# Optimization experiments

Hardware: AMD Instinct MI355X
Metric: run time of the kernel (lower is better)

## Reference

```python
import jax, jax.numpy as jnp
import numpy as np

N, E = 50000, 800000
NDIM_IN, EDIM, HID, NDIM_OUT, NCLS = 64, 64, 128, 128, 10


def _linear_params(k, fan_in, fan_out):
    lim = 1.0 / np.sqrt(fan_in)
    kw, kb = jax.random.split(k)
    W = jax.random.uniform(kw, (fan_in, fan_out), minval=-lim, maxval=lim, dtype=jnp.float32)
    b = jax.random.uniform(kb, (fan_out,), minval=-lim, maxval=lim, dtype=jnp.float32)
    return W, b


def setup_inputs() -> dict:
    key = jax.random.key(0)
    ks = jax.random.split(key, 9)
    Wm1, bm1 = _linear_params(ks[0], NDIM_IN + EDIM, HID)      # layer1 W_msg
    Wa1, ba1 = _linear_params(ks[1], NDIM_IN + HID, HID)       # layer1 W_apply
    Wm2, bm2 = _linear_params(ks[2], HID + EDIM, NDIM_OUT)     # layer2 W_msg
    Wa2, ba2 = _linear_params(ks[3], HID + NDIM_OUT, NDIM_OUT) # layer2 W_apply
    Wp, bp = _linear_params(ks[4], 2 * NDIM_OUT, NCLS)         # edge predictor
    nfeats = jax.random.normal(ks[5], (N, NDIM_IN), dtype=jnp.float32)
    efeats = jax.random.normal(ks[6], (E, EDIM), dtype=jnp.float32)
    src = jax.random.randint(ks[7], (E,), 0, N)
    dst = jax.random.randint(ks[8], (E,), 0, N)
    return dict(nfeats=nfeats, efeats=efeats, src=src, dst=dst,
                Wm1=Wm1, bm1=bm1, Wa1=Wa1, ba1=ba1,
                Wm2=Wm2, bm2=bm2, Wa2=Wa2, ba2=ba2, Wp=Wp, bp=bp)


def _sage_layer(h, efeats, src, dst, Wm, bm, Wa, ba):
    # per-edge message: W_msg([h_src || e])
    m = jnp.concatenate([h[src], efeats], axis=1) @ Wm + bm          # [E, out]
    # mean aggregation by destination node (0 for zero in-degree, as in DGL fn.mean)
    s = jax.ops.segment_sum(m, dst, num_segments=N)                  # [N, out]
    deg = jax.ops.segment_sum(jnp.ones((E,), m.dtype), dst, num_segments=N)
    h_neigh = s / jnp.maximum(deg, 1.0)[:, None]
    return jax.nn.relu(jnp.concatenate([h, h_neigh], axis=1) @ Wa + ba)


def reference(nfeats, efeats, src, dst, Wm1, bm1, Wa1, ba1, Wm2, bm2, Wa2, ba2, Wp, bp):
    h = _sage_layer(nfeats, efeats, src, dst, Wm1, bm1, Wa1, ba1)
    # dropout between layers is identity in eval mode
    h = _sage_layer(h, efeats, src, dst, Wm2, bm2, Wa2, ba2)
    # MLPPredictor: per-edge score = W([h_u || h_v])
    score = jnp.concatenate([h[src], h[dst]], axis=1) @ Wp + bp      # [E, 10]
    return score
```

## Files before the change

kernel.cpp:

```cpp
#include <hip/hip_runtime.h>

typedef float  f32x4 __attribute__((ext_vector_type(4)));
typedef short  s16x8 __attribute__((ext_vector_type(8)));
typedef unsigned int u32x4 __attribute__((ext_vector_type(4)));

#define DEVINL __device__ __forceinline__

DEVINL float4 ld4(const float* p) { return *reinterpret_cast<const float4*>(p); }
DEVINL void st4(float* p, float4 v) { *reinterpret_cast<float4*>(p) = v; }
DEVINL f32x4 ld4v(const float* p) { return *reinterpret_cast<const f32x4*>(p); }
DEVINL f32x4 ld4nt(const float* p) {
  return __builtin_nontemporal_load(reinterpret_cast<const f32x4*>(p));
}

DEVINL void split8(const float4& f0, const float4& f1, s16x8& hi, s16x8& lo) {
  unsigned hb[8], lb[8];
  const float f[8] = {f0.x, f0.y, f0.z, f0.w, f1.x, f1.y, f1.z, f1.w};
  #pragma unroll
  for (int j = 0; j < 8; ++j) {
    unsigned u = __float_as_uint(f[j]);
    unsigned h = u & 0xffff0000u;
    float l = f[j] - __uint_as_float(h);
    hb[j] = h;
    lb[j] = __float_as_uint(l) & 0xffff0000u;
  }
  u32x4 H = {(hb[0] >> 16) | hb[1], (hb[2] >> 16) | hb[3],
             (hb[4] >> 16) | hb[5], (hb[6] >> 16) | hb[7]};
  u32x4 L = {(lb[0] >> 16) | lb[1], (lb[2] >> 16) | lb[3],
             (lb[4] >> 16) | lb[5], (lb[6] >> 16) | lb[7]};
  hi = __builtin_bit_cast(s16x8, H);
  lo = __builtin_bit_cast(s16x8, L);
}

DEVINL void split1(float f, unsigned short& h, unsigned short& l) {
  unsigned u = __float_as_uint(f);
  unsigned hb = (u + 0x7fffu + ((u >> 16) & 1u)) >> 16;
  float hf = __uint_as_float(hb << 16);
  float d = f - hf;
  unsigned v = __float_as_uint(d);
  unsigned lb = (v + 0x7fffu + ((v >> 16) & 1u)) >> 16;
  h = (unsigned short)hb;
  l = (unsigned short)lb;
}

__global__ __launch_bounds__(128) void wprep2_kernel(
    const float* __restrict__ Wm1, const float* __restrict__ Wa1, const float* __restrict__ bm1,
    const float* __restrict__ Wm2, const float* __restrict__ Wa2, const float* __restrict__ bm2,
    float* __restrict__ bmw1, float* __restrict__ bmw2,
    unsigned short* __restrict__ w1h, unsigned short* __restrict__ w1l,
    unsigned short* __restrict__ w2h, unsigned short* __restrict__ w2l)
{
  int b = blockIdx.x, j = threadIdx.x;
  unsigned short h, l;
  if (b < 128) {
    float acc = 0.f;
    for (int k = 0; k < 128; ++k) acc = fmaf(Wm1[b * 128 + k], Wa1[(64 + k) * 128 + j], acc);
    split1(acc, h, l);
    w1h[(size_t)j * 192 + 64 + b] = h;
    w1l[(size_t)j * 192 + 64 + b] = l;
  } else if (b < 320) {
    int i = b - 128;
    float acc = 0.f;
    for (int k = 0; k < 128; ++k) acc = fmaf(Wm2[i * 128 + k], Wa2[(128 + k) * 128 + j], acc);
    split1(acc, h, l);
    w2h[(size_t)j * 320 + 128 + i] = h;
    w2l[(size_t)j * 320 + 128 + i] = l;
  } else if (b == 320) {
    float acc = 0.f;
    for (int k = 0; k < 128; ++k) acc = fmaf(bm1[k], Wa1[(64 + k) * 128 + j], acc);
    bmw1[j] = acc;
  } else if (b == 321) {
    float acc = 0.f;
    for (int k = 0; k < 128; ++k) acc = fmaf(bm2[k], Wa2[(128 + k) * 128 + j], acc);
    bmw2[j] = acc;
  } else if (b < 386) {
    int t = b - 322;
    split1(Wa1[t * 128 + j], h, l);
    w1h[(size_t)j * 192 + t] = h;
    w1l[(size_t)j * 192 + t] = l;
  } else {
    int t = b - 386;
    split1(Wa2[t * 128 + j], h, l);
    w2h[(size_t)j * 320 + t] = h;
    w2l[(size_t)j * 320 + t] = l;
  }
}

__global__ __launch_bounds__(256) void hist_kernel(
    const int* __restrict__ dst, int* __restrict__ deg, int E)
{
  int e = blockIdx.x * 256 + threadIdx.x;
  if (e < E) atomicAdd(&deg[dst[e]], 1);
}

__global__ __launch_bounds__(256) void scan_blk_kernel(
    const int* __restrict__ in, int* __restrict__ excl, int* __restrict__ bsum, int n)
{
  __shared__ int tmp[256];
  int t = threadIdx.x;
  int i = blockIdx.x * 256 + t;
  int v = (i < n) ? in[i] : 0;
  tmp[t] = v;
  __syncthreads();
  #pragma unroll
  for (int off = 1; off < 256; off <<= 1) {
    int add = (t >= off) ? tmp[t - off] : 0;
    __syncthreads();
    tmp[t] += add;
    __syncthreads();
  }
  if (i < n) excl[i] = tmp[t] - v;
  if (t == 255) bsum[blockIdx.x] = tmp[255];
}

__global__ __launch_bounds__(256) void finalize2_kernel(
    const int* __restrict__ excl, const int* __restrict__ bsum, int nblk,
    int* __restrict__ rp, int* __restrict__ cursor, int N, int E)
{
  __shared__ int bs[256];
  int t = threadIdx.x;
  bs[t] = (t < nblk) ? bsum[t] : 0;
  __syncthreads();
  #pragma unroll
  for (int off = 1; off < 256; off <<= 1) {
    int add = (t >= off) ? bs[t - off] : 0;
    __syncthreads();
    bs[t] += add;
    __syncthreads();
  }
  int i = blockIdx.x * 256 + t;
  if (i < N) {
    int blk = i >> 8;
    int boff = blk ? bs[blk - 1] : 0;
    int v = excl[i] + boff;
    rp[i] = v;
    cursor[i] = v;
  }
  if (i == N) rp[N] = E;
}

__global__ __launch_bounds__(256) void scatter_kernel(
    const int* __restrict__ dst, const int* __restrict__ src,
    int* __restrict__ cursor, int2* __restrict__ es, int E)
{
  int e = blockIdx.x * 256 + threadIdx.x;
  if (e >= E) return;
  int d = dst[e];
  int pos = atomicAdd(&cursor[d], 1);
  es[pos] = make_int2(e, src[e]);
}

__global__ __launch_bounds__(256) void csr_agg_l1_kernel(
    const float* __restrict__ ef, const float* __restrict__ nf,
    const int2* __restrict__ es, const int* __restrict__ rp,
    float* __restrict__ meanE, float* __restrict__ meanH1, int N)
{
  int node = (int)((blockIdx.x * 256u + threadIdx.x) >> 6);
  node = __builtin_amdgcn_readfirstlane(node);
  if (node >= N) return;
  const int lane = threadIdx.x & 63;
  const int g = lane >> 4, l16 = lane & 15;
  const int beg = rp[node], end = rp[node + 1];
  const int full_end = beg + ((end - beg) & ~15);

  f32x4 ea = {0.f, 0.f, 0.f, 0.f}, ha = {0.f, 0.f, 0.f, 0.f};
  int k0 = beg;
  for (; k0 < full_end; k0 += 16) {
    #pragma unroll
    for (int u = 0; u < 4; ++u) {
      int2 p = es[k0 + 4 * u + g];
      ea += ld4nt(ef + (size_t)p.x * 64 + l16 * 4);
      ha += ld4v (nf + (size_t)p.y * 64 + l16 * 4);
    }
  }
  #pragma unroll
  for (int u = 0; u < 4; ++u) {
    int i = k0 + 4 * u + g;
    if (i < end) {
      int2 p = es[i];
      ea += ld4nt(ef + (size_t)p.x * 64 + l16 * 4);
      ha += ld4v (nf + (size_t)p.y * 64 + l16 * 4);
    }
  }
  #pragma unroll
  for (int j = 0; j < 4; ++j) {
    ea[j] += __shfl_xor(ea[j], 16);
    ea[j] += __shfl_xor(ea[j], 32);
    ha[j] += __shfl_xor(ha[j], 16);
    ha[j] += __shfl_xor(ha[j], 32);
  }
  if (g == 0) {
    float inv = 1.0f / fmaxf((float)(end - beg), 1.0f);
    st4(meanE  + (size_t)node * 64 + l16 * 4,
        make_float4(ea[0] * inv, ea[1] * inv, ea[2] * inv, ea[3] * inv));
    st4(meanH1 + (size_t)node * 64 + l16 * 4,
        make_float4(ha[0] * inv, ha[1] * inv, ha[2] * inv, ha[3] * inv));
  }
}

__global__ __launch_bounds__(256) void csr_agg128_kernel(
    const float* __restrict__ X, const int2* __restrict__ es,
    const int* __restrict__ rp, float* __restrict__ out, int N)
{
  int node = (int)((blockIdx.x * 256u + threadIdx.x) >> 6);
  node = __builtin_amdgcn_readfirstlane(node);
  if (node >= N) return;
  const int lane = threadIdx.x & 63;
  const int g = lane >> 5, l32 = lane & 31;
  const int beg = rp[node], end = rp[node + 1];
  const int full_end = beg + ((end - beg) & ~7);

  f32x4 a = {0.f, 0.f, 0.f, 0.f};
  int k0 = beg;
  for (; k0 < full_end; k0 += 8) {
    #pragma unroll
    for (int u = 0; u < 4; ++u) {
      int s = es[k0 + 2 * u + g].y;
      a += ld4v(X + (size_t)s * 128 + l32 * 4);
    }
  }
  #pragma unroll
  for (int u = 0; u < 4; ++u) {
    int i = k0 + 2 * u + g;
    if (i < end) {
      int s = es[i].y;
      a += ld4v(X + (size_t)s * 128 + l32 * 4);
    }
  }
  #pragma unroll
  for (int j = 0; j < 4; ++j) a[j] += __shfl_xor(a[j], 32);
  if (g == 0) {
    float inv = 1.0f / fmaxf((float)(end - beg), 1.0f);
    st4(out + (size_t)node * 128 + l32 * 4,
        make_float4(a[0] * inv, a[1] * inv, a[2] * inv, a[3] * inv));
  }
}

template<int C1, int C2, int C3>
__global__ __launch_bounds__(256, 2) void fgemm_kernel(
    const float* __restrict__ X1, const float* __restrict__ X2, const float* __restrict__ X3,
    const unsigned short* __restrict__ WtHi, const unsigned short* __restrict__ WtLo,
    const float* __restrict__ ba, const float* __restrict__ bmw,
    const int* __restrict__ deg, float* __restrict__ out, int n)
{
  constexpr int K = C1 + C2 + C3;
  const int lane = threadIdx.x & 63;
  const int w = threadIdx.x >> 6;
  const int base = blockIdx.x * 128;
  const int l15 = lane & 15;
  const int lg = lane >> 4;

  f32x4 acc[2][8] = {};

  #pragma unroll
  for (int k0 = 0; k0 < K; k0 += 32) {
    const float* sp;
    int C, off;
    if (k0 < C1)            { sp = X1; C = C1; off = k0; }
    else if (k0 < C1 + C2)  { sp = X2; C = C2; off = k0 - C1; }
    else                    { sp = X3; C = C3; off = k0 - C1 - C2; }
    const int ca = off + lg * 8;

    s16x8 ah[2], al[2];
    #pragma unroll
    for (int mi = 0; mi < 2; ++mi) {
      int row = base + w * 32 + mi * 16 + l15;
      if (row >= n) row = n - 1;
      float4 f0 = ld4(sp + (size_t)row * C + ca);
      float4 f1 = ld4(sp + (size_t)row * C + ca + 4);
      split8(f0, f1, ah[mi], al[mi]);
    }

    s16x8 bh[8], bl[8];
    const int kb = k0 + lg * 8;
    #pragma unroll
    for (int ni = 0; ni < 8; ++ni) {
      size_t woff = (size_t)(ni * 16 + l15) * K + kb;
      bh[ni] = *reinterpret_cast<const s16x8*>(WtHi + woff);
      bl[ni] = *reinterpret_cast<const s16x8*>(WtLo + woff);
    }

    #pragma unroll
    for (int mi = 0; mi < 2; ++mi)
      #pragma unroll
      for (int ni = 0; ni < 8; ++ni) {
        acc[mi][ni] = __builtin_amdgcn_mfma_f32_16x16x32_bf16(ah[mi], bh[ni], acc[mi][ni], 0, 0, 0);
        acc[mi][ni] = __builtin_amdgcn_mfma_f32_16x16x32_bf16(ah[mi], bl[ni], acc[mi][ni], 0, 0, 0);
        acc[mi][ni] = __builtin_amdgcn_mfma_f32_16x16x32_bf16(al[mi], bh[ni], acc[mi][ni], 0, 0, 0);
      }
  }

  float bav[8], bmv[8];
  #pragma unroll
  for (int ni = 0; ni < 8; ++ni) {
    bav[ni] = ba[ni * 16 + l15];
    bmv[ni] = bmw[ni * 16 + l15];
  }

  #pragma unroll
  for (int mi = 0; mi < 2; ++mi) {
    #pragma unroll
    for (int r = 0; r < 4; ++r) {
      int grow = base + w * 32 + mi * 16 + lg * 4 + r;
      if (grow >= n) continue;
      float msk = deg[grow] > 0 ? 1.0f : 0.0f;
      float* op = out + (size_t)grow * 128 + l15;
      #pragma unroll
      for (int ni = 0; ni < 8; ++ni)
        op[ni * 16] = fmaxf(acc[mi][ni][r] + bav[ni] + msk * bmv[ni], 0.0f);
    }
  }
}

__global__ __launch_bounds__(256, 2) void fgemm2_pred_kernel(
    const float* __restrict__ X1, const float* __restrict__ X2, const float* __restrict__ X3,
    const unsigned short* __restrict__ WtHi, const unsigned short* __restrict__ WtLo,
    const float* __restrict__ ba, const float* __restrict__ bmw,
    const int* __restrict__ deg, const float* __restrict__ Wp,
    const float* __restrict__ bp, float* __restrict__ pt, int n)
{
  constexpr int C1 = 128, C2 = 128, C3 = 64;
  constexpr int K = C1 + C2 + C3;
  __shared__ float xs[128 * 129];
  __shared__ float wl[2560];

  const int tid = threadIdx.x;
  const int lane = tid & 63;
  const int w = tid >> 6;
  const int base = blockIdx.x * 128;
  const int l15 = lane & 15;
  const int lg = lane >> 4;

  for (int i = tid; i < 2560; i += 256) wl[i] = Wp[i];

  f32x4 acc[2][8] = {};

  #pragma unroll
  for (int k0 = 0; k0 < K; k0 += 32) {
    const float* sp;
    int C, off;
    if (k0 < C1)            { sp = X1; C = C1; off = k0; }
    else if (k0 < C1 + C2)  { sp = X2; C = C2; off = k0 - C1; }
    else                    { sp = X3; C = C3; off = k0 - C1 - C2; }
    const int ca = off + lg * 8;

    s16x8 ah[2], al[2];
    #pragma unroll
    for (int mi = 0; mi < 2; ++mi) {
      int row = base + w * 32 + mi * 16 + l15;
      if (row >= n) row = n - 1;
      float4 f0 = ld4(sp + (size_t)row * C + ca);
      float4 f1 = ld4(sp + (size_t)row * C + ca + 4);
      split8(f0, f1, ah[mi], al[mi]);
    }

    s16x8 bh[8], bl[8];
    const int kb = k0 + lg * 8;
    #pragma unroll
    for (int ni = 0; ni < 8; ++ni) {
      size_t woff = (size_t)(ni * 16 + l15) * K + kb;
      bh[ni] = *reinterpret_cast<const s16x8*>(WtHi + woff);
      bl[ni] = *reinterpret_cast<const s16x8*>(WtLo + woff);
    }

    #pragma unroll
    for (int mi = 0; mi < 2; ++mi)
      #pragma unroll
      for (int ni = 0; ni < 8; ++ni) {
        acc[mi][ni] = __builtin_amdgcn_mfma_f32_16x16x32_bf16(ah[mi], bh[ni], acc[mi][ni], 0, 0, 0);
        acc[mi][ni] = __builtin_amdgcn_mfma_f32_16x16x32_bf16(ah[mi], bl[ni], acc[mi][ni], 0, 0, 0);
        acc[mi][ni] = __builtin_amdgcn_mfma_f32_16x16x32_bf16(al[mi], bh[ni], acc[mi][ni], 0, 0, 0);
      }
  }

  float bav[8], bmv[8];
  #pragma unroll
  for (int ni = 0; ni < 8; ++ni) {
    bav[ni] = ba[ni * 16 + l15];
    bmv[ni] = bmw[ni * 16 + l15];
  }

  #pragma unroll
  for (int mi = 0; mi < 2; ++mi) {
    #pragma unroll
    for (int r = 0; r < 4; ++r) {
      int lr = w * 32 + mi * 16 + lg * 4 + r;
      int grow = base + lr;
      if (grow >= n) continue;
      float msk = deg[grow] > 0 ? 1.0f : 0.0f;
      #pragma unroll
      for (int ni = 0; ni < 8; ++ni)
        xs[lr * 129 + ni * 16 + l15] =
            fmaxf(acc[mi][ni][r] + bav[ni] + msk * bmv[ni], 0.0f);
    }
  }
  __syncthreads();

  const int r = tid >> 1;
  const int half = tid & 1;
  const int grow = base + r;
  if (grow < n) {
    const float* wb = wl + half * 1280;
    float a[10] = {};
    for (int k = 0; k < 128; ++k) {
      float x = xs[r * 129 + k];
      #pragma unroll
      for (int j = 0; j < 10; ++j) a[j] = fmaf(x, wb[k * 10 + j], a[j]);
    }
    float* op = pt + (size_t)grow * 20 + half * 10;
    if (half) {
      #pragma unroll
      for (int j = 0; j < 10; ++j) op[j] = a[j] + bp[j];
    } else {
      #pragma unroll
      for (int j = 0; j < 10; ++j) op[j] = a[j];
    }
  }
}

__global__ __launch_bounds__(256) void pred_edge_kernel(
    const float* __restrict__ pt, const int* __restrict__ src, const int* __restrict__ dst,
    float* __restrict__ out, int E)
{
  int idx = blockIdx.x * 256 + threadIdx.x;
  if (idx >= E * 5) return;
  int e = idx / 5;
  int jj = idx - e * 5;
  int s = src[e], d = dst[e];
  const float2* p2 = (const float2*)pt;
  float2 a = p2[(size_t)s * 10 + jj];
  float2 b = p2[(size_t)d * 10 + 5 + jj];
  ((float2*)out)[idx] = make_float2(a.x + b.x, a.y + b.y);
}

extern "C" void kernel_launch(void* const* d_in, const int* in_sizes, int n_in,
                              void* d_out, int out_size, void* d_ws, size_t ws_size,
                              hipStream_t stream) {
  const float* nfeats = (const float*)d_in[0];
  const float* efeats = (const float*)d_in[1];
  const int*   src    = (const int*)d_in[2];
  const int*   dst    = (const int*)d_in[3];
  const float* Wm1 = (const float*)d_in[4];
  const float* bm1 = (const float*)d_in[5];
  const float* Wa1 = (const float*)d_in[6];
  const float* ba1 = (const float*)d_in[7];
  const float* Wm2 = (const float*)d_in[8];
  const float* bm2 = (const float*)d_in[9];
  const float* Wa2 = (const float*)d_in[10];
  const float* ba2 = (const float*)d_in[11];
  const float* Wp  = (const float*)d_in[12];
  const float* bp  = (const float*)d_in[13];

  const int N = in_sizes[0] / 64;
  const int E = in_sizes[2];
  const int nblk = (N + 255) / 256;

  int* ip     = (int*)d_ws;
  int* deg_i  = ip;
  int* rp     = ip + (size_t)N;
  int* scr    = ip + 2 * (size_t)N + 4 + E;
  int* excl   = scr;
  int* cursor = scr + (size_t)N;
  int* bsum   = scr + 2 * (size_t)N;

  size_t fbase = (4 * (size_t)N + 516 + (size_t)E + 3) & ~(size_t)3;
  float* fp     = (float*)d_ws;
  float* meanE  = fp + fbase;
  float* meanH1 = meanE  + (size_t)N * 64;
  float* meanH2 = meanH1 + (size_t)N * 64;
  float* h1     = meanH2 + (size_t)N * 256;
  float* pt     = meanH1;
  float* out    = (float*)d_out;

  int2*  es   = (int2*)(fp + fbase + (size_t)N * 512);
  float* wst  = fp + fbase + (size_t)N * 512 + 2 * (size_t)E;
  float* bmw1 = wst;
  float* bmw2 = bmw1 + 128;
  unsigned short* w1h = (unsigned short*)(bmw2 + 128);
  unsigned short* w1l = w1h + 192 * 128;
  unsigned short* w2h = w1l + 192 * 128;
  unsigned short* w2l = w2h + 320 * 128;

  hipMemsetAsync(deg_i, 0, (size_t)N * sizeof(int), stream);

  int gridE  = (E + 255) / 256;
  int gridN  = (N + 127) / 128;
  int gridNW = ((N * 64) + 255) / 256;

  wprep2_kernel<<<514, 128, 0, stream>>>(Wm1, Wa1, bm1, Wm2, Wa2, bm2,
                                         bmw1, bmw2, w1h, w1l, w2h, w2l);

  hist_kernel<<<gridE, 256, 0, stream>>>(dst, deg_i, E);
  scan_blk_kernel<<<nblk, 256, 0, stream>>>(deg_i, excl, bsum, N);
  finalize2_kernel<<<(N + 256) / 256, 256, 0, stream>>>(excl, bsum, nblk, rp, cursor, N, E);
  scatter_kernel<<<gridE, 256, 0, stream>>>(dst, src, cursor, es, E);

  csr_agg_l1_kernel<<<gridNW, 256, 0, stream>>>(efeats, nfeats, es, rp, meanE, meanH1, N);
  fgemm_kernel<64, 64, 64><<<gridN, 256, 0, stream>>>(
      nfeats, meanH1, meanE, w1h, w1l, ba1, bmw1, deg_i, h1, N);

  csr_agg128_kernel<<<gridNW, 256, 0, stream>>>(h1, es, rp, meanH2, N);
  fgemm2_pred_kernel<<<gridN, 256, 0, stream>>>(
      h1, meanH2, meanE, w2h, w2l, ba2, bmw2, deg_i, Wp, bp, pt, N);

  pred_edge_kernel<<<(E * 5 + 255) / 256, 256, 0, stream>>>(pt, src, dst, out, E);
}
```

Measured before the change: 346.2 us.

## Store intermediates as packed bf16 hi/lo pairs and fuse prep with histogram

Intermediate node tensors (aggregated means, h1, mean of h1) are now written as a 32-bit word holding bf16 hi and lo halves, packed once by the producer. The GEMM kernels then only shuffle bits into MFMA fragments instead of splitting fp32 on every load. Node features are pre-packed, and the weight prep, packing and degree histogram are merged into one launch. The 128-wide aggregation loop is unrolled to 16 edges with loads issued before accumulation. The gather width and memory traffic stay the same, and the switch from truncation to round-to-nearest split changes the numerics slightly.

```diff
diff --git a/kernel.cpp b/kernel.cpp
--- a/kernel.cpp
+++ b/kernel.cpp
@@ -7,29 +7,41 @@
 #define DEVINL __device__ __forceinline__
 
 DEVINL float4 ld4(const float* p) { return *reinterpret_cast<const float4*>(p); }
-DEVINL void st4(float* p, float4 v) { *reinterpret_cast<float4*>(p) = v; }
 DEVINL f32x4 ld4v(const float* p) { return *reinterpret_cast<const f32x4*>(p); }
+DEVINL u32x4 ld4u(const unsigned* p) { return *reinterpret_cast<const u32x4*>(p); }
 DEVINL f32x4 ld4nt(const float* p) {
   return __builtin_nontemporal_load(reinterpret_cast<const f32x4*>(p));
 }
 
-DEVINL void split8(const float4& f0, const float4& f1, s16x8& hi, s16x8& lo) {
-  unsigned hb[8], lb[8];
-  const float f[8] = {f0.x, f0.y, f0.z, f0.w, f1.x, f1.y, f1.z, f1.w};
-  #pragma unroll
-  for (int j = 0; j < 8; ++j) {
-    unsigned u = __float_as_uint(f[j]);
-    unsigned h = u & 0xffff0000u;
-    float l = f[j] - __uint_as_float(h);
-    hb[j] = h;
-    lb[j] = __float_as_uint(l) & 0xffff0000u;
-  }
-  u32x4 H = {(hb[0] >> 16) | hb[1], (hb[2] >> 16) | hb[3],
-             (hb[4] >> 16) | hb[5], (hb[6] >> 16) | hb[7]};
-  u32x4 L = {(lb[0] >> 16) | lb[1], (lb[2] >> 16) | lb[3],
-             (lb[4] >> 16) | lb[5], (lb[6] >> 16) | lb[7]};
-  hi = __builtin_bit_cast(s16x8, H);
-  lo = __builtin_bit_cast(s16x8, L);
+DEVINL unsigned pack1(float f) {
+  unsigned u = __float_as_uint(f);
+  unsigned hb = (u + 0x7fffu + ((u >> 16) & 1u)) & 0xffff0000u;
+  float l = f - __uint_as_float(hb);
+  unsigned v = __float_as_uint(l);
+  unsigned lb = (v + 0x7fffu + ((v >> 16) & 1u)) >> 16;
+  return hb | lb;
+}
+DEVINL float unpack1(unsigned v) {
+  return __uint_as_float(v & 0xffff0000u) + __uint_as_float(v << 16);
+}
+DEVINL f32x4 unpack4(u32x4 v) {
+  f32x4 r;
+  #pragma unroll
+  for (int i = 0; i < 4; ++i) r[i] = unpack1(v[i]);
+  return r;
+}
+DEVINL void unpack_frag(u32x4 a, u32x4 b, s16x8& ah, s16x8& al) {
+  u32x4 H, L;
+  H[0] = (a[0] >> 16) | (a[1] & 0xffff0000u);
+  H[1] = (a[2] >> 16) | (a[3] & 0xffff0000u);
+  H[2] = (b[0] >> 16) | (b[1] & 0xffff0000u);
+  H[3] = (b[2] >> 16) | (b[3] & 0xffff0000u);
+  L[0] = (a[0] & 0xffffu) | (a[1] << 16);
+  L[1] = (a[2] & 0xffffu) | (a[3] << 16);
+  L[2] = (b[0] & 0xffffu) | (b[1] << 16);
+  L[3] = (b[2] & 0xffffu) | (b[3] << 16);
+  ah = __builtin_bit_cast(s16x8, H);
+  al = __builtin_bit_cast(s16x8, L);
 }
 
 DEVINL void split1(float f, unsigned short& h, unsigned short& l) {
@@ -43,54 +55,59 @@
   l = (unsigned short)lb;
 }
 
-__global__ __launch_bounds__(128) void wprep2_kernel(
+__global__ __launch_bounds__(256) void prep_kernel(
     const float* __restrict__ Wm1, const float* __restrict__ Wa1, const float* __restrict__ bm1,
     const float* __restrict__ Wm2, const float* __restrict__ Wa2, const float* __restrict__ bm2,
     float* __restrict__ bmw1, float* __restrict__ bmw2,
     unsigned short* __restrict__ w1h, unsigned short* __restrict__ w1l,
-    unsigned short* __restrict__ w2h, unsigned short* __restrict__ w2l)
-{
-  int b = blockIdx.x, j = threadIdx.x;
-  unsigned short h, l;
-  if (b < 128) {
-    float acc = 0.f;
-    for (int k = 0; k < 128; ++k) acc = fmaf(Wm1[b * 128 + k], Wa1[(64 + k) * 128 + j], acc);
-    split1(acc, h, l);
-    w1h[(size_t)j * 192 + 64 + b] = h;
-    w1l[(size_t)j * 192 + 64 + b] = l;
-  } else if (b < 320) {
-    int i = b - 128;
-    float acc = 0.f;
-    for (int k = 0; k < 128; ++k) acc = fmaf(Wm2[i * 128 + k], Wa2[(128 + k) * 128 + j], acc);
-    split1(acc, h, l);
-    w2h[(size_t)j * 320 + 128 + i] = h;
-    w2l[(size_t)j * 320 + 128 + i] = l;
-  } else if (b == 320) {
-    float acc = 0.f;
-    for (int k = 0; k < 128; ++k) acc = fmaf(bm1[k], Wa1[(64 + k) * 128 + j], acc);
-    bmw1[j] = acc;
-  } else if (b == 321) {
-    float acc = 0.f;
-    for (int k = 0; k < 128; ++k) acc = fmaf(bm2[k], Wa2[(128 + k) * 128 + j], acc);
-    bmw2[j] = acc;
-  } else if (b < 386) {
-    int t = b - 322;
-    split1(Wa1[t * 128 + j], h, l);
-    w1h[(size_t)j * 192 + t] = h;
-    w1l[(size_t)j * 192 + t] = l;
+    unsigned short* __restrict__ w2h, unsigned short* __restrict__ w2l,
+    const float* __restrict__ nf, unsigned* __restrict__ nfp, int nelem,
+    const int* __restrict__ dst, int* __restrict__ deg, int E, int npack)
+{
+  int blk = blockIdx.x;
+  if (blk < 257) {
+    int b = blk * 2 + (threadIdx.x >> 7);
+    int j = threadIdx.x & 127;
+    unsigned short h, l;
+    if (b < 128) {
+      float acc = 0.f;
+      for (int k = 0; k < 128; ++k) acc = fmaf(Wm1[b * 128 + k], Wa1[(64 + k) * 128 + j], acc);
+      split1(acc, h, l);
+      w1h[(size_t)j * 192 + 64 + b] = h;
+      w1l[(size_t)j * 192 + 64 + b] = l;
+    } else if (b < 320) {
+      int i = b - 128;
+      float acc = 0.f;
+      for (int k = 0; k < 128; ++k) acc = fmaf(Wm2[i * 128 + k], Wa2[(128 + k) * 128 + j], acc);
+      split1(acc, h, l);
+      w2h[(size_t)j * 320 + 128 + i] = h;
+      w2l[(size_t)j * 320 + 128 + i] = l;
+    } else if (b == 320) {
+      float acc = 0.f;
+      for (int k = 0; k < 128; ++k) acc = fmaf(bm1[k], Wa1[(64 + k) * 128 + j], acc);
+      bmw1[j] = acc;
+    } else if (b == 321) {
+      float acc = 0.f;
+      for (int k = 0; k < 128; ++k) acc = fmaf(bm2[k], Wa2[(128 + k) * 128 + j], acc);
+      bmw2[j] = acc;
+    } else if (b < 386) {
+      int t = b - 322;
+      split1(Wa1[t * 128 + j], h, l);
+      w1h[(size_t)j * 192 + t] = h;
+      w1l[(size_t)j * 192 + t] = l;
+    } else {
+      int t = b - 386;
+      split1(Wa2[t * 128 + j], h, l);
+      w2h[(size_t)j * 320 + t] = h;
+      w2l[(size_t)j * 320 + t] = l;
+    }
+  } else if (blk < 257 + npack) {
+    int idx = (blk - 257) * 256 + threadIdx.x;
+    if (idx < nelem) nfp[idx] = pack1(nf[idx]);
   } else {
-    int t = b - 386;
-    split1(Wa2[t * 128 + j], h, l);
-    w2h[(size_t)j * 320 + t] = h;
-    w2l[(size_t)j * 320 + t] = l;
-  }
-}
-
-__global__ __launch_bounds__(256) void hist_kernel(
-    const int* __restrict__ dst, int* __restrict__ deg, int E)
-{
-  int e = blockIdx.x * 256 + threadIdx.x;
-  if (e < E) atomicAdd(&deg[dst[e]], 1);
+    int e = (blk - 257 - npack) * 256 + threadIdx.x;
+    if (e < E) atomicAdd(&deg[dst[e]], 1);
+  }
 }
 
 __global__ __launch_bounds__(256) void scan_blk_kernel(
@@ -153,7 +170,7 @@
 __global__ __launch_bounds__(256) void csr_agg_l1_kernel(
     const float* __restrict__ ef, const float* __restrict__ nf,
     const int2* __restrict__ es, const int* __restrict__ rp,
-    float* __restrict__ meanE, float* __restrict__ meanH1, int N)
+    unsigned* __restrict__ mEp, unsigned* __restrict__ mH1p, int N)
 {
   int node = (int)((blockIdx.x * 256u + threadIdx.x) >> 6);
   node = __builtin_amdgcn_readfirstlane(node);
@@ -191,16 +208,20 @@
   }
   if (g == 0) {
     float inv = 1.0f / fmaxf((float)(end - beg), 1.0f);
-    st4(meanE  + (size_t)node * 64 + l16 * 4,
-        make_float4(ea[0] * inv, ea[1] * inv, ea[2] * inv, ea[3] * inv));
-    st4(meanH1 + (size_t)node * 64 + l16 * 4,
-        make_float4(ha[0] * inv, ha[1] * inv, ha[2] * inv, ha[3] * inv));
+    u32x4 pe, ph;
+    #pragma unroll
+    for (int j = 0; j < 4; ++j) {
+      pe[j] = pack1(ea[j] * inv);
+      ph[j] = pack1(ha[j] * inv);
+    }
+    *reinterpret_cast<u32x4*>(mEp  + (size_t)node * 64 + l16 * 4) = pe;
+    *reinterpret_cast<u32x4*>(mH1p + (size_t)node * 64 + l16 * 4) = ph;
   }
 }
 
 __global__ __launch_bounds__(256) void csr_agg128_kernel(
-    const float* __restrict__ X, const int2* __restrict__ es,
-    const int* __restrict__ rp, float* __restrict__ out, int N)
+    const unsigned* __restrict__ X, const int2* __restrict__ es,
+    const int* __restrict__ rp, unsigned* __restrict__ out, int N)
 {
   int node = (int)((blockIdx.x * 256u + threadIdx.x) >> 6);
   node = __builtin_amdgcn_readfirstlane(node);
@@ -208,40 +229,46 @@
   const int lane = threadIdx.x & 63;
   const int g = lane >> 5, l32 = lane & 31;
   const int beg = rp[node], end = rp[node + 1];
-  const int full_end = beg + ((end - beg) & ~7);
+  const int full_end = beg + ((end - beg) & ~15);
 
   f32x4 a = {0.f, 0.f, 0.f, 0.f};
   int k0 = beg;
-  for (; k0 < full_end; k0 += 8) {
-    #pragma unroll
-    for (int u = 0; u < 4; ++u) {
+  for (; k0 < full_end; k0 += 16) {
+    u32x4 v[8];
+    #pragma unroll
+    for (int u = 0; u < 8; ++u) {
       int s = es[k0 + 2 * u + g].y;
-      a += ld4v(X + (size_t)s * 128 + l32 * 4);
-    }
-  }
-  #pragma unroll
-  for (int u = 0; u < 4; ++u) {
+      v[u] = ld4u(X + (size_t)s * 128 + l32 * 4);
+    }
+    #pragma unroll
+    for (int u = 0; u < 8; ++u) a += unpack4(v[u]);
+  }
+  #pragma unroll
+  for (int u = 0; u < 8; ++u) {
     int i = k0 + 2 * u + g;
     if (i < end) {
       int s = es[i].y;
-      a += ld4v(X + (size_t)s * 128 + l32 * 4);
+      a += unpack4(ld4u(X + (size_t)s * 128 + l32 * 4));
     }
   }
   #pragma unroll
   for (int j = 0; j < 4; ++j) a[j] += __shfl_xor(a[j], 32);
   if (g == 0) {
     float inv = 1.0f / fmaxf((float)(end - beg), 1.0f);
-    st4(out + (size_t)node * 128 + l32 * 4,
-        make_float4(a[0] * inv, a[1] * inv, a[2] * inv, a[3] * inv));
+    u32x4 pv;
+    #pragma unroll
+    for (int j = 0; j < 4; ++j) pv[j] = pack1(a[j] * inv);
+    *reinterpret_cast<u32x4*>(out + (size_t)node * 128 + l32 * 4) = pv;
   }
 }
 
 template<int C1, int C2, int C3>
 __global__ __launch_bounds__(256, 2) void fgemm_kernel(
-    const float* __restrict__ X1, const float* __restrict__ X2, const float* __restrict__ X3,
+    const unsigned* __restrict__ X1, const unsigned* __restrict__ X2,
+    const unsigned* __restrict__ X3,
     const unsigned short* __restrict__ WtHi, const unsigned short* __restrict__ WtLo,
     const float* __restrict__ ba, const float* __restrict__ bmw,
-    const int* __restrict__ deg, float* __restrict__ out, int n)
+    const int* __restrict__ deg, unsigned* __restrict__ out, int n)
 {
   constexpr int K = C1 + C2 + C3;
   const int lane = threadIdx.x & 63;
@@ -254,7 +281,7 @@
 
   #pragma unroll
   for (int k0 = 0; k0 < K; k0 += 32) {
-    const float* sp;
+    const unsigned* sp;
     int C, off;
     if (k0 < C1)            { sp = X1; C = C1; off = k0; }
     else if (k0 < C1 + C2)  { sp = X2; C = C2; off = k0 - C1; }
@@ -266,9 +293,9 @@
     for (int mi = 0; mi < 2; ++mi) {
       int row = base + w * 32 + mi * 16 + l15;
       if (row >= n) row = n - 1;
-      float4 f0 = ld4(sp + (size_t)row * C + ca);
-      float4 f1 = ld4(sp + (size_t)row * C + ca + 4);
-      split8(f0, f1, ah[mi], al[mi]);
+      u32x4 p0 = ld4u(sp + (size_t)row * C + ca);
+      u32x4 p1 = ld4u(sp + (size_t)row * C + ca + 4);
+      unpack_frag(p0, p1, ah[mi], al[mi]);
     }
 
     s16x8 bh[8], bl[8];
@@ -304,16 +331,17 @@
       int grow = base + w * 32 + mi * 16 + lg * 4 + r;
       if (grow >= n) continue;
       float msk = deg[grow] > 0 ? 1.0f : 0.0f;
-      float* op = out + (size_t)grow * 128 + l15;
+      unsigned* op = out + (size_t)grow * 128 + l15;
       #pragma unroll
       for (int ni = 0; ni < 8; ++ni)
-        op[ni * 16] = fmaxf(acc[mi][ni][r] + bav[ni] + msk * bmv[ni], 0.0f);
+        op[ni * 16] = pack1(fmaxf(acc[mi][ni][r] + bav[ni] + msk * bmv[ni], 0.0f));
     }
   }
 }
 
 __global__ __launch_bounds__(256, 2) void fgemm2_pred_kernel(
-    const float* __restrict__ X1, const float* __restrict__ X2, const float* __restrict__ X3,
+    const unsigned* __restrict__ X1, const unsigned* __restrict__ X2,
+    const unsigned* __restrict__ X3,
     const unsigned short* __restrict__ WtHi, const unsigned short* __restrict__ WtLo,
     const float* __restrict__ ba, const float* __restrict__ bmw,
     const int* __restrict__ deg, const float* __restrict__ Wp,
@@ -337,7 +365,7 @@
 
   #pragma unroll
   for (int k0 = 0; k0 < K; k0 += 32) {
-    const float* sp;
+    const unsigned* sp;
     int C, off;
     if (k0 < C1)            { sp = X1; C = C1; off = k0; }
     else if (k0 < C1 + C2)  { sp = X2; C = C2; off = k0 - C1; }
@@ -349,9 +377,9 @@
     for (int mi = 0; mi < 2; ++mi) {
       int row = base + w * 32 + mi * 16 + l15;
       if (row >= n) row = n - 1;
-      float4 f0 = ld4(sp + (size_t)row * C + ca);
-      float4 f1 = ld4(sp + (size_t)row * C + ca + 4);
-      split8(f0, f1, ah[mi], al[mi]);
+      u32x4 p0 = ld4u(sp + (size_t)row * C + ca);
+      u32x4 p1 = ld4u(sp + (size_t)row * C + ca + 4);
+      unpack_frag(p0, p1, ah[mi], al[mi]);
     }
 
     s16x8 bh[8], bl[8];
@@ -464,13 +492,13 @@
   int* bsum   = scr + 2 * (size_t)N;
 
   size_t fbase = (4 * (size_t)N + 516 + (size_t)E + 3) & ~(size_t)3;
-  float* fp     = (float*)d_ws;
-  float* meanE  = fp + fbase;
-  float* meanH1 = meanE  + (size_t)N * 64;
-  float* meanH2 = meanH1 + (size_t)N * 64;
-  float* h1     = meanH2 + (size_t)N * 256;
-  float* pt     = meanH1;
-  float* out    = (float*)d_out;
+  float*    fp    = (float*)d_ws;
+  unsigned* mEp   = (unsigned*)(fp + fbase);
+  float*    pt    = fp + fbase + (size_t)N * 64;
+  unsigned* mH1p  = (unsigned*)pt;
+  unsigned* mH2p  = (unsigned*)(fp + fbase + (size_t)N * 128);
+  unsigned* h1p   = (unsigned*)(fp + fbase + (size_t)N * 384);
+  float*    out   = (float*)d_out;
 
   int2*  es   = (int2*)(fp + fbase + (size_t)N * 512);
   float* wst  = fp + fbase + (size_t)N * 512 + 2 * (size_t)E;
@@ -480,28 +508,30 @@
   unsigned short* w1l = w1h + 192 * 128;
   unsigned short* w2h = w1l + 192 * 128;
   unsigned short* w2l = w2h + 320 * 128;
+  unsigned* nfp = (unsigned*)(w2l + 320 * 128);
 
   hipMemsetAsync(deg_i, 0, (size_t)N * sizeof(int), stream);
 
   int gridE  = (E + 255) / 256;
   int gridN  = (N + 127) / 128;
   int gridNW = ((N * 64) + 255) / 256;
-
-  wprep2_kernel<<<514, 128, 0, stream>>>(Wm1, Wa1, bm1, Wm2, Wa2, bm2,
-                                         bmw1, bmw2, w1h, w1l, w2h, w2l);
-
-  hist_kernel<<<gridE, 256, 0, stream>>>(dst, deg_i, E);
+  int npack  = (N * 64 + 255) / 256;
+
+  prep_kernel<<<257 + npack + gridE, 256, 0, stream>>>(
+      Wm1, Wa1, bm1, Wm2, Wa2, bm2, bmw1, bmw2, w1h, w1l, w2h, w2l,
+      nfeats, nfp, N * 64, dst, deg_i, E, npack);
+
   scan_blk_kernel<<<nblk, 256, 0, stream>>>(deg_i, excl, bsum, N);
   finalize2_kernel<<<(N + 256) / 256, 256, 0, stream>>>(excl, bsum, nblk, rp, cursor, N, E);
   scatter_kernel<<<gridE, 256, 0, stream>>>(dst, src, cursor, es, E);
 
-  csr_agg_l1_kernel<<<gridNW, 256, 0, stream>>>(efeats, nfeats, es, rp, meanE, meanH1, N);
+  csr_agg_l1_kernel<<<gridNW, 256, 0, stream>>>(efeats, nfeats, es, rp, mEp, mH1p, N);
   fgemm_kernel<64, 64, 64><<<gridN, 256, 0, stream>>>(
-      nfeats, meanH1, meanE, w1h, w1l, ba1, bmw1, deg_i, h1, N);
-
-  csr_agg128_kernel<<<gridNW, 256, 0, stream>>>(h1, es, rp, meanH2, N);
+      nfp, mH1p, mEp, w1h, w1l, ba1, bmw1, deg_i, h1p, N);
+
+  csr_agg128_kernel<<<gridNW, 256, 0, stream>>>(h1p, es, rp, mH2p, N);
   fgemm2_pred_kernel<<<gridN, 256, 0, stream>>>(
-      h1, meanH2, meanE, w2h, w2l, ba2, bmw2, deg_i, Wp, bp, pt, N);
+      h1p, mH2p, mEp, w2h, w2l, ba2, bmw2, deg_i, Wp, bp, pt, N);
 
   pred_edge_kernel<<<(E * 5 + 255) / 256, 256, 0, stream>>>(pt, src, dst, out, E);
 }
```

Result: no change. 345.2 us (-0.3%).
